# Kernel optimization log

Hardware: AMD Instinct MI355X
Metric: run time of the kernel (lower is better)

The kernel has to match this reference:

```python
import jax, jax.numpy as jnp
from jax import lax
import numpy as np

B, S, E, HID = 16, 7, 64, 64
RES = (64, 64); D = RES[0] * RES[1]
XLOW, XHIGH = -0.5, 0.5
RLOW, RHIGH = float(np.sqrt(0.01)), float(np.sqrt(0.05))
PIXEL_MULT = 1.0; N_ITER = 3; TSOFT = 1.0 / float(np.sqrt(E))

def _build_grid():
    ranges = [np.linspace(XLOW, XHIGH, r) for r in RES]
    g = np.stack(np.meshgrid(*ranges, indexing='xy'), axis=-1)
    g = g.reshape(RES[0], RES[1], -1).reshape(1, -1, 2)
    return jnp.asarray(g, dtype=jnp.float32)

ABS_GRID = _build_grid()  # [1, D, 2]

def _ln(x, g, b):
    m = jnp.mean(x, -1, keepdims=True)
    v = jnp.mean(jnp.square(x - m), -1, keepdims=True)
    return (x - m) * lax.rsqrt(v + 1e-5) * g + b

def _forward(data, slot_noise, pos_rand, conv0_w, conv0_b, conv1_w, conv1_b, conv2_w, conv2_b,
             dataN_g, dataN_b, queryN_g, queryN_b, toK_w, toK_b, toV_w, toV_b, dense_w, dense_b,
             mlp1_w, mlp1_b, mlp2_w, mlp2_b, gru_wih, gru_whh, gru_bih, gru_bhh,
             alpha1_w, alpha1_b, alpha2_w, alpha2_b, final1_w, final1_b, final2_w, final2_b,
             slots_mu, slots_logsigma):
    dn = ('NCHW', 'OIHW', 'NCHW')
    def conv(x, w, b):
        return lax.conv_general_dilated(x, w, (1, 1), 'SAME', dimension_numbers=dn) + b[None, :, None, None]
    # CNN encoder: Conv-ReLU x3, 'same' padding, k=5
    x = jax.nn.relu(conv(data, conv0_w, conv0_b))
    x = jax.nn.relu(conv(x, conv1_w, conv1_b))
    x = jax.nn.relu(conv(x, conv2_w, conv2_b))
    enc = x.transpose(0, 2, 3, 1).reshape(B, D, HID)
    enc = _ln(enc, dataN_g, dataN_b)

    queries = slots_mu + jnp.exp(slots_logsigma) * slot_noise  # [B,S,E]
    # init_slots: faithful replication (source indexes the SLOT dim, and swaps rlow/rhigh)
    pos_scale = pos_rand.at[:, :2, :].add(-0.5)
    pos_scale = pos_scale.at[:, -1, :].set((RLOW - RHIGH) * pos_rand[:, -1, :] + RHIGH)

    encK = enc @ toK_w + toK_b  # [B,D,E]
    encV = enc @ toV_w + toV_b

    def init_mlp(y):
        y = _ln(y, queryN_g, queryN_b)
        return jax.nn.relu(y @ mlp1_w + mlp1_b) @ mlp2_w + mlp2_b

    def get_kv(ps):
        # per-slot relative grid: [B,S,D,2]
        rel = (ABS_GRID[:, None] - ps[:, :, None, :2]) / ps[:, :, -1][:, :, None, None]
        eg = PIXEL_MULT * (rel @ dense_w + dense_b)  # [B,S,D,E]
        return init_mlp(encK[:, None] + eg), init_mlp(encV[:, None] + eg)

    def att_wts(q, k):
        logits = jnp.einsum('bse,bsde->bsd', q, k) * TSOFT
        att = jax.nn.softmax(logits, axis=1)  # softmax over slots
        wts = att / jnp.sum(att, -1, keepdims=True) + 1e-8
        return att, wts

    def update_frames(wts):
        new_pos = jnp.einsum('bsd,de->bse', wts, ABS_GRID[0])  # [B,S,2]
        d2 = jnp.sum(jnp.square(ABS_GRID[:, None] - new_pos[:, :, None]), -1)  # [B,S,D]
        new_scale = jnp.sqrt(jnp.einsum('bsd,bsd->bs', wts, d2))
        return jnp.concatenate([new_pos, new_scale[..., None]], -1)

    def gru(xg, h):
        gi = xg @ gru_wih.T + gru_bih
        gh = h @ gru_whh.T + gru_bhh
        ir, iz, inn = jnp.split(gi, 3, -1)
        hr, hz, hn = jnp.split(gh, 3, -1)
        r = jax.nn.sigmoid(ir + hr)
        z = jax.nn.sigmoid(iz + hz)
        n = jnp.tanh(inn + r * hn)
        return (1.0 - z) * n + z * h

    for _ in range(N_ITER):
        keys, vals = get_kv(pos_scale)
        att, wts = att_wts(_ln(queries, queryN_g, queryN_b), keys)
        pos_scale = update_frames(wts)
        upd = jnp.einsum('bsd,bsde->bse', wts, vals)
        queries = gru(upd.reshape(-1, E), queries.reshape(-1, E)).reshape(B, S, E)

    keys, _ = get_kv(pos_scale)
    att, wts = att_wts(_ln(queries, queryN_g, queryN_b), keys)
    nps = update_frames(wts)
    alpha = jax.nn.sigmoid(jax.nn.relu(queries @ alpha1_w + alpha1_b) @ alpha2_w + alpha2_b)
    slot_feat = jax.nn.relu(queries @ final1_w + final1_b) @ final2_w + final2_b + nps
    return queries, att, slot_feat, alpha

def setup_inputs() -> dict:
    ks = jax.random.split(jax.random.key(0), 20)
    f32 = jnp.float32
    def rn(i, shape, s):
        return jax.random.normal(ks[i], shape, f32) * s
    inp = dict(
        data=jax.random.normal(ks[0], (B, 1, RES[0], RES[1]), f32),
        slot_noise=jax.random.normal(ks[1], (B, S, E), f32),
        pos_rand=jax.random.uniform(ks[2], (B, S, 3), dtype=f32),
        conv0_w=rn(3, (HID, 1, 5, 5), 0.2), conv0_b=jnp.zeros(HID, f32),
        conv1_w=rn(4, (HID, HID, 5, 5), 0.025), conv1_b=jnp.zeros(HID, f32),
        conv2_w=rn(5, (HID, HID, 5, 5), 0.025), conv2_b=jnp.zeros(HID, f32),
        dataN_g=jnp.ones(HID, f32), dataN_b=jnp.zeros(HID, f32),
        queryN_g=jnp.ones(E, f32), queryN_b=jnp.zeros(E, f32),
        toK_w=rn(6, (HID, E), 0.125), toK_b=jnp.zeros(E, f32),
        toV_w=rn(7, (HID, E), 0.125), toV_b=jnp.zeros(E, f32),
        dense_w=rn(8, (2, E), 0.7), dense_b=jnp.zeros(E, f32),
        mlp1_w=rn(9, (E, E), 0.125), mlp1_b=jnp.zeros(E, f32),
        mlp2_w=rn(10, (E, E), 0.125), mlp2_b=jnp.zeros(E, f32),
        gru_wih=rn(11, (3 * E, E), 0.125), gru_whh=rn(12, (3 * E, E), 0.125),
        gru_bih=jnp.zeros(3 * E, f32), gru_bhh=jnp.zeros(3 * E, f32),
        alpha1_w=rn(13, (E, 32), 0.125), alpha1_b=jnp.zeros(32, f32),
        alpha2_w=rn(14, (32, 1), 0.18), alpha2_b=jnp.zeros(1, f32),
        final1_w=rn(15, (E, HID), 0.125), final1_b=jnp.zeros(HID, f32),
        final2_w=rn(16, (HID, 3), 0.125), final2_b=jnp.zeros(3, f32),
        slots_mu=rn(17, (1, 1, E), 1.0),
        slots_logsigma=rn(18, (1, 1, E), 0.01),
    )
    return inp

def reference(data, slot_noise, pos_rand, conv0_w, conv0_b, conv1_w, conv1_b, conv2_w, conv2_b,
              dataN_g, dataN_b, queryN_g, queryN_b, toK_w, toK_b, toV_w, toV_b, dense_w, dense_b,
              mlp1_w, mlp1_b, mlp2_w, mlp2_b, gru_wih, gru_whh, gru_bih, gru_bhh,
              alpha1_w, alpha1_b, alpha2_w, alpha2_b, final1_w, final1_b, final2_w, final2_b,
              slots_mu, slots_logsigma):
    return _forward(data, slot_noise, pos_rand, conv0_w, conv0_b, conv1_w, conv1_b, conv2_w, conv2_b,
                    dataN_g, dataN_b, queryN_g, queryN_b, toK_w, toK_b, toV_w, toV_b, dense_w, dense_b,
                    mlp1_w, mlp1_b, mlp2_w, mlp2_b, gru_wih, gru_whh, gru_bih, gru_bhh,
                    alpha1_w, alpha1_b, alpha2_w, alpha2_b, final1_w, final1_b, final2_w, final2_b,
                    slots_mu, slots_logsigma)
```

## Files before the change

kernel.cpp:

```cpp
#include <hip/hip_runtime.h>
#include <cmath>


#define RLOW_F 0.1f
#define RHIGH_F 0.22360679774997896f
#define W0CONST 1.00004096f
#define SR2 704.3386243f

typedef __attribute__((ext_vector_type(8))) __bf16 bf16x8;
typedef __attribute__((ext_vector_type(4))) float f32x4;

__device__ __forceinline__ float wsum64(float v){
  #pragma unroll
  for (int off = 32; off > 0; off >>= 1) v += __shfl_xor(v, off, 64);
  return v;
}
__device__ __forceinline__ float rdlane(float v, int l){
  return __int_as_float(__builtin_amdgcn_readlane(__float_as_int(v), l));
}
__device__ __forceinline__ unsigned short bf16bits(float v){
  __bf16 h = (__bf16)v;
  return *reinterpret_cast<unsigned short*>(&h);
}

__device__ __forceinline__ void pp_core(int row, int e, float qv,
    float px, float py, float sc,
    const float* __restrict__ qg_, const float* __restrict__ qb_,
    const float* __restrict__ dw, const float* __restrict__ db,
    const float* __restrict__ mlp2w, const float* __restrict__ mlp2b,
    float* __restrict__ absc, float* __restrict__ w2qc){
  float m = wsum64(qv) * (1.f/64.f);
  float d = qv - m;
  float var = wsum64(d*d) * (1.f/64.f);
  float qlnv = d * (1.0f/sqrtf(var + 1e-5f)) * qg_[e] + qb_[e];
  float A  = dw[e]      / sc;
  float Bv = dw[64 + e] / sc;
  absc[row*192 + e]       = A;
  absc[row*192 + 64 + e]  = Bv;
  absc[row*192 + 128 + e] = db[e] - px*A - py*Bv;
  float acc = 0.f;
  const float* wrow = mlp2w + e*64;
  for (int j = 0; j < 64; j++) acc = fmaf(wrow[j], rdlane(qlnv, j), acc);
  w2qc[row*68 + e] = acc;
  float c2 = wsum64(mlp2b[e] * qlnv);
  if (e == 0) w2qc[row*68 + 64] = c2;
}

__global__ void k_prep(const float* __restrict__ noise, const float* __restrict__ prand,
                       const float* __restrict__ mu, const float* __restrict__ logsig,
                       const float* __restrict__ qg_, const float* __restrict__ qb_,
                       const float* __restrict__ dw, const float* __restrict__ db,
                       const float* __restrict__ mlp2w, const float* __restrict__ mlp2b,
                       float* __restrict__ queries, float* __restrict__ ps,
                       float* __restrict__ absc, float* __restrict__ w2qc,
                       float* __restrict__ accF, float* __restrict__ upd){
  int row = blockIdx.x;
  int e = threadIdx.x;
  int s = row % 7;
  float qv = mu[e] + expf(logsig[e]) * noise[row*64 + e];
  queries[row*64 + e] = qv;
  upd[row*64 + e] = 0.f;
  if (e < 4) accF[row*4 + e] = 0.f;
  float pv = 0.f;
  if (e < 3){
    float pr = prand[row*3 + e];
    if (s < 2)       pv = pr - 0.5f;
    else if (s == 6) pv = (RLOW_F - RHIGH_F)*pr + RHIGH_F;
    else             pv = pr;
    ps[row*3 + e] = pv;
  }
  float px = rdlane(pv, 0), py = rdlane(pv, 1), sc = rdlane(pv, 2);
  pp_core(row, e, qv, px, py, sc, qg_, qb_, dw, db, mlp2w, mlp2b, absc, w2qc);
}

__global__ __launch_bounds__(256) void k_conv0(const float* __restrict__ in,
                        const float* __restrict__ w, const float* __restrict__ bias,
                        unsigned short* __restrict__ out){
  int bi = blockIdx.x; int b = bi >> 6; int y = bi & 63;
  int t = threadIdx.x; int lane = t & 63; int xg = t >> 6;
  __shared__ float s_in[5*68];
  __shared__ float s_w[64*25];
  __shared__ float s_out[64*65];
  for (int i = t; i < 1600; i += 256) s_w[i] = w[i];
  for (int i = t; i < 340; i += 256){
    int r = i / 68, cx = i % 68;
    int yy = y + r - 2, gx = cx - 2;
    float v = 0.f;
    if (yy >= 0 && yy < 64 && gx >= 0 && gx < 64) v = in[(b*64 + yy)*64 + gx];
    s_in[r*68 + cx] = v;
  }
  __syncthreads();
  int o = lane;
  float bvv = bias[o];
  float acc[16];
  #pragma unroll
  for (int k = 0; k < 16; k++) acc[k] = bvv;
  #pragma unroll
  for (int ky = 0; ky < 5; ky++){
    float rv[20];
    const float4* p = reinterpret_cast<const float4*>(&s_in[ky*68 + xg*16]);
    #pragma unroll
    for (int q = 0; q < 5; q++){ float4 f = p[q]; rv[q*4]=f.x; rv[q*4+1]=f.y; rv[q*4+2]=f.z; rv[q*4+3]=f.w; }
    #pragma unroll
    for (int kx = 0; kx < 5; kx++){
      float wv = s_w[o*25 + ky*5 + kx];
      #pragma unroll
      for (int k = 0; k < 16; k++) acc[k] = fmaf(rv[k+kx], wv, acc[k]);
    }
  }
  #pragma unroll
  for (int k = 0; k < 16; k++) s_out[o*65 + xg*16 + k] = fmaxf(acc[k], 0.f);
  __syncthreads();
  for (int i = t; i < 4096; i += 256){
    int px = i >> 6, ch = i & 63;
// ... 127 lines not shown
  int n = nt*16 + cr;
  out[idx] = bf16bits(w1[k*64 + n]);
}

__global__ __launch_bounds__(256) void k_projm(const float* __restrict__ enc,
                       const unsigned short* __restrict__ kpack, const float* __restrict__ bk,
                       const unsigned short* __restrict__ vpack, const float* __restrict__ bvp,
                       unsigned short* __restrict__ K, unsigned short* __restrict__ V){
  int bi = blockIdx.x; int b = bi >> 6; int tile = bi & 63;
  int t = threadIdx.x; int wv = t >> 6; int l = t & 63;
  int q = l >> 4, cr = l & 15;
  int d0 = tile*64 + wv*16;

  const bf16x8* kp = reinterpret_cast<const bf16x8*>(kpack);
  const bf16x8* vp = reinterpret_cast<const bf16x8*>(vpack);
  bf16x8 KB[8], VB[8];
  #pragma unroll
  for (int f = 0; f < 8; f++){ KB[f] = kp[f*64 + l]; VB[f] = vp[f*64 + l]; }

  const float* er = enc + (size_t)(b*4096 + d0 + cr)*64;
  bf16x8 a0, a1;
  #pragma unroll
  for (int h = 0; h < 2; h++){
    const float4* e4 = reinterpret_cast<const float4*>(er + (h ? (32 + q*8) : (q*8)));
    #pragma unroll
    for (int p = 0; p < 2; p++){
      float4 e = e4[p];
      if (h == 0){ a0[p*4+0]=(__bf16)e.x; a0[p*4+1]=(__bf16)e.y; a0[p*4+2]=(__bf16)e.z; a0[p*4+3]=(__bf16)e.w; }
      else       { a1[p*4+0]=(__bf16)e.x; a1[p*4+1]=(__bf16)e.y; a1[p*4+2]=(__bf16)e.z; a1[p*4+3]=(__bf16)e.w; }
    }
  }

  f32x4 zero = {0.f,0.f,0.f,0.f};
  f32x4 aK[4], aV[4];
  #pragma unroll
  for (int nt = 0; nt < 4; nt++){
    aK[nt] = __builtin_amdgcn_mfma_f32_16x16x32_bf16(a0, KB[nt],     zero,   0, 0, 0);
    aK[nt] = __builtin_amdgcn_mfma_f32_16x16x32_bf16(a1, KB[4 + nt], aK[nt], 0, 0, 0);
    aV[nt] = __builtin_amdgcn_mfma_f32_16x16x32_bf16(a0, VB[nt],     zero,   0, 0, 0);
    aV[nt] = __builtin_amdgcn_mfma_f32_16x16x32_bf16(a1, VB[4 + nt], aV[nt], 0, 0, 0);
  }
  #pragma unroll
  for (int nt = 0; nt < 4; nt++){
    float bkv = bk[nt*16 + cr], bvv = bvp[nt*16 + cr];
    #pragma unroll
    for (int reg = 0; reg < 4; reg++){
      size_t base = ((size_t)b*4096 + d0 + q*4 + reg)*64 + nt*16 + cr;
      K[base] = bf16bits(aK[nt][reg] + bkv);
      V[base] = bf16bits(aV[nt][reg] + bvv);
    }
  }
}

__global__ __launch_bounds__(256) void k_attnK(const unsigned short* __restrict__ encX,
     const unsigned short* __restrict__ w1pack, const float* __restrict__ mlp1b,
     const float* __restrict__ absc, const float* __restrict__ qg_,
     const float* __restrict__ qb_, const float* __restrict__ w2qc,
     float* __restrict__ att, float* __restrict__ accF){
  int bi = blockIdx.x;
  int b = bi >> 6, tile = bi & 63;
  int t = threadIdx.x; int wv = t >> 6; int l = t & 63;
  int q = l >> 4, cr = l & 15;
  int m0 = tile*64 + wv*16;
  int drow = m0 + cr;

  __shared__ float s_log[7*64];
  __shared__ float s_absc[7*192];
  __shared__ float s_wq[7*68];
  __shared__ unsigned short s_w1[4096];
  for (int i = t; i < 1344; i += 256) s_absc[i] = absc[b*7*192 + i];
  for (int i = t; i < 476;  i += 256) s_wq[i]   = w2qc[b*7*68 + i];
  {
    const uint4* g = reinterpret_cast<const uint4*>(w1pack);
    uint4* d = reinterpret_cast<uint4*>(s_w1);
    for (int i = t; i < 512; i += 256) d[i] = g[i];
  }

  const unsigned short* er = encX + (size_t)(b*4096 + drow)*64;
  float gx = -0.5f + (float)(drow & 63) * (1.f/63.f);
  float gy = -0.5f + (float)((drow >> 6) & 63) * (1.f/63.f);
  float xb[16], gq[16], bq[16];
  {
    bf16x8 ea = *reinterpret_cast<const bf16x8*>(er + q*8);
    bf16x8 eb = *reinterpret_cast<const bf16x8*>(er + 32 + q*8);
    #pragma unroll
    for (int i = 0; i < 8; i++){ xb[i] = (float)ea[i]; xb[8+i] = (float)eb[i]; }
  }
  #pragma unroll
  for (int h = 0; h < 2; h++){
    int fb = h ? (32 + q*8) : (q*8);
    const float4* g4 = reinterpret_cast<const float4*>(qg_ + fb);
    const float4* b4 = reinterpret_cast<const float4*>(qb_ + fb);
    #pragma unroll
    for (int p = 0; p < 2; p++){
      float4 gg = g4[p], bb = b4[p];
      int o = h*8 + p*4;
      gq[o+0]=gg.x; gq[o+1]=gg.y; gq[o+2]=gg.z; gq[o+3]=gg.w;
      bq[o+0]=bb.x; bq[o+1]=bb.y; bq[o+2]=bb.z; bq[o+3]=bb.w;
    }
  }
  float b1v[4];
  #pragma unroll
  for (int nt = 0; nt < 4; nt++) b1v[nt] = mlp1b[nt*16 + cr];
  __syncthreads();

  const bf16x8* wl = reinterpret_cast<const bf16x8*>(s_w1);
  f32x4 zero = {0.f, 0.f, 0.f, 0.f};

  for (int sp = 0; sp < 4; sp++){
    int s0 = sp*2;
    int np = (sp == 3) ? 1 : 2;
    int sB = (np == 2) ? s0 + 1 : s0;
    float x0[16], x1[16];
    float s1a = 0.f, s2a = 0.f, s1b = 0.f, s2b = 0.f;
    {
      const float* Ac = s_absc + s0*192;
      #pragma unroll
      for (int h = 0; h < 2; h++){
        int fb = h ? (32 + q*8) : (q*8);
        const float4* A4 = reinterpret_cast<const float4*>(Ac + fb);
        const float4* B4 = reinterpret_cast<const float4*>(Ac + 64 + fb);
        const float4* C4 = reinterpret_cast<const float4*>(Ac + 128 + fb);
        #pragma unroll
        for (int p = 0; p < 2; p++){
          float4 Av = A4[p], Bv = B4[p], Cv = C4[p];
          int o = h*8 + p*4;
          x0[o+0] = xb[o+0] + gx*Av.x + gy*Bv.x + Cv.x;
          x0[o+1] = xb[o+1] + gx*Av.y + gy*Bv.y + Cv.y;
          x0[o+2] = xb[o+2] + gx*Av.z + gy*Bv.z + Cv.z;
          x0[o+3] = xb[o+3] + gx*Av.w + gy*Bv.w + Cv.w;
        }
// ... 47 lines not shown
      bf16x8 w1f = wl[(4 + nt)*64 + l];
      acc0[nt] = __builtin_amdgcn_mfma_f32_16x16x32_bf16(a00, w0,  zero,     0, 0, 0);
      acc0[nt] = __builtin_amdgcn_mfma_f32_16x16x32_bf16(a01, w1f, acc0[nt], 0, 0, 0);
      acc1[nt] = __builtin_amdgcn_mfma_f32_16x16x32_bf16(a10, w0,  zero,     0, 0, 0);
      acc1[nt] = __builtin_amdgcn_mfma_f32_16x16x32_bf16(a11, w1f, acc1[nt], 0, 0, 0);
    }

    float p0[4] = {0.f,0.f,0.f,0.f}, p1[4] = {0.f,0.f,0.f,0.f};
    #pragma unroll
    for (int nt = 0; nt < 4; nt++){
      float wq0 = s_wq[s0*68 + nt*16 + cr];
      float wq1 = s_wq[sB*68 + nt*16 + cr];
      #pragma unroll
      for (int reg = 0; reg < 4; reg++){
        p0[reg] = fmaf(fmaxf(acc0[nt][reg] + b1v[nt], 0.f), wq0, p0[reg]);
        p1[reg] = fmaf(fmaxf(acc1[nt][reg] + b1v[nt], 0.f), wq1, p1[reg]);
      }
    }
    #pragma unroll
    for (int off = 1; off < 16; off <<= 1){
      #pragma unroll
      for (int reg = 0; reg < 4; reg++){
        p0[reg] += __shfl_xor(p0[reg], off, 64);
        p1[reg] += __shfl_xor(p1[reg], off, 64);
      }
    }
    if (cr == 0){
      float c20 = s_wq[s0*68 + 64];
      float c21 = s_wq[sB*68 + 64];
      #pragma unroll
      for (int reg = 0; reg < 4; reg++){
        s_log[s0*64 + wv*16 + q*4 + reg] = (p0[reg] + c20) * 0.125f;
        if (np == 2) s_log[sB*64 + wv*16 + q*4 + reg] = (p1[reg] + c21) * 0.125f;
      }
    }
  }
  __syncthreads();

  if (t < 64){
    float lv[7];
    #pragma unroll
    for (int s = 0; s < 7; s++) lv[s] = s_log[s*64 + t];
    float mx = lv[0];
    #pragma unroll
    for (int s = 1; s < 7; s++) mx = fmaxf(mx, lv[s]);
    float sm = 0.f;
    #pragma unroll
    for (int s = 0; s < 7; s++){ lv[s] = expf(lv[s] - mx); sm += lv[s]; }
    float inv = 1.0f / sm;
    #pragma unroll
    for (int s = 0; s < 7; s++){
      float a = lv[s] * inv;
      s_log[s*64 + t] = a;
      att[(size_t)(b*7+s)*4096 + tile*64 + t] = a;
    }
  }
  __syncthreads();

  if (t < 224){
    int s = t >> 5, r = t & 31;
    float a1 = s_log[s*64 + r];
    float a2 = s_log[s*64 + r + 32];
    float gx1 = -0.5f + (float)r * (1.f/63.f);
    float gx2 = -0.5f + (float)(r + 32) * (1.f/63.f);
    float gyc = -0.5f + (float)tile * (1.f/63.f);
    float gy2c = gyc*gyc;
    float w0 = a1 + a2;
    float w1 = a1*gx1 + a2*gx2;
    float w2 = w0*gyc;
    float w3 = a1*(gx1*gx1 + gy2c) + a2*(gx2*gx2 + gy2c);
    #pragma unroll
    for (int m = 1; m < 32; m <<= 1){
      w0 += __shfl_xor(w0, m, 64);
      w1 += __shfl_xor(w1, m, 64);
      w2 += __shfl_xor(w2, m, 64);
      w3 += __shfl_xor(w3, m, 64);
    }
    if (r == 0){
      atomicAdd(&accF[(b*7+s)*4 + 0], w0);
      atomicAdd(&accF[(b*7+s)*4 + 1], w1);
      atomicAdd(&accF[(b*7+s)*4 + 2], w2);
      atomicAdd(&accF[(b*7+s)*4 + 3], w3);
    }
  }
}

__global__ __launch_bounds__(256) void k_attnV(const unsigned short* __restrict__ encX,
     const unsigned short* __restrict__ w1pack, const float* __restrict__ mlp1b,
     const float* __restrict__ absc, const float* __restrict__ qg_,
     const float* __restrict__ qb_, const float* __restrict__ att,
     const float* __restrict__ accF, float* __restrict__ upd){
  int bi = blockIdx.x;
  int b = bi >> 6, tile = bi & 63;
  int t = threadIdx.x; int wv = t >> 6; int l = t & 63;
  int q = l >> 4, cr = l & 15;
  int m0 = tile*64 + wv*16;
  int drow = m0 + cr;

  __shared__ float s_absc[7*192];
  __shared__ float s_att[7*64];
  __shared__ float s_upd[7*64];
  __shared__ float s_inv[7];
  __shared__ unsigned short s_w1[4096];
  for (int i = t; i < 1344; i += 256) s_absc[i] = absc[b*7*192 + i];
  for (int i = t; i < 448;  i += 256){
    s_att[i] = att[(size_t)(b*7 + (i >> 6))*4096 + tile*64 + (i & 63)];
    s_upd[i] = 0.f;
  }
  if (t < 7) s_inv[t] = 1.0f / accF[(b*7 + t)*4];
  {
    const uint4* g = reinterpret_cast<const uint4*>(w1pack);
    uint4* d = reinterpret_cast<uint4*>(s_w1);
    for (int i = t; i < 512; i += 256) d[i] = g[i];
  }

  const unsigned short* er = encX + (size_t)(b*4096 + drow)*64;
  float gx = -0.5f + (float)(drow & 63) * (1.f/63.f);
  float gy = -0.5f + (float)((drow >> 6) & 63) * (1.f/63.f);
  float xb[16], gq[16], bq[16];
  {
    bf16x8 ea = *reinterpret_cast<const bf16x8*>(er + q*8);
    bf16x8 eb = *reinterpret_cast<const bf16x8*>(er + 32 + q*8);
    #pragma unroll
    for (int i = 0; i < 8; i++){ xb[i] = (float)ea[i]; xb[8+i] = (float)eb[i]; }
  }
  #pragma unroll
  for (int h = 0; h < 2; h++){
    int fb = h ? (32 + q*8) : (q*8);
    const float4* g4 = reinterpret_cast<const float4*>(qg_ + fb);
    const float4* b4 = reinterpret_cast<const float4*>(qb_ + fb);
    #pragma unroll
    for (int p = 0; p < 2; p++){
      float4 gg = g4[p], bb = b4[p];
      int o = h*8 + p*4;
      gq[o+0]=gg.x; gq[o+1]=gg.y; gq[o+2]=gg.z; gq[o+3]=gg.w;
      bq[o+0]=bb.x; bq[o+1]=bb.y; bq[o+2]=bb.z; bq[o+3]=bb.w;
    }
  }
  float b1v[4];
  #pragma unroll
  for (int nt = 0; nt < 4; nt++) b1v[nt] = mlp1b[nt*16 + cr];
  __syncthreads();

  const bf16x8* wl = reinterpret_cast<const bf16x8*>(s_w1);
  f32x4 zero = {0.f, 0.f, 0.f, 0.f};

  for (int sp = 0; sp < 4; sp++){
    int s0 = sp*2;
    int np = (sp == 3) ? 1 : 2;
    int sB = (np == 2) ? s0 + 1 : s0;
    float x0[16], x1[16];
    float s1a = 0.f, s2a = 0.f, s1b = 0.f, s2b = 0.f;
    {
      const float* Ac = s_absc + s0*192;
      #pragma unroll
      for (int h = 0; h < 2; h++){
        int fb = h ? (32 + q*8) : (q*8);
        const float4* A4 = reinterpret_cast<const float4*>(Ac + fb);
        const float4* B4 = reinterpret_cast<const float4*>(Ac + 64 + fb);
        const float4* C4 = reinterpret_cast<const float4*>(Ac + 128 + fb);
        #pragma unroll
        for (int p = 0; p < 2; p++){
          float4 Av = A4[p], Bv = B4[p], Cv = C4[p];
          int o = h*8 + p*4;
          x0[o+0] = xb[o+0] + gx*Av.x + gy*Bv.x + Cv.x;
          x0[o+1] = xb[o+1] + gx*Av.y + gy*Bv.y + Cv.y;
          x0[o+2] = xb[o+2] + gx*Av.z + gy*Bv.z + Cv.z;
          x0[o+3] = xb[o+3] + gx*Av.w + gy*Bv.w + Cv.w;
        }
      }
      #pragma unroll
      for (int k = 0; k < 16; k++){ s1a += x0[k]; s2a = fmaf(x0[k], x0[k], s2a); }
    }
    {
      const float* Ac = s_absc + sB*192;
      #pragma unroll
      for (int h = 0; h < 2; h++){
        int fb = h ? (32 + q*8) : (q*8);
        const float4* A4 = reinterpret_cast<const float4*>(Ac + fb);
        const float4* B4 = reinterpret_cast<const float4*>(Ac + 64 + fb);
        const float4* C4 = reinterpret_cast<const float4*>(Ac + 128 + fb);
        #pragma unroll
        for (int p = 0; p < 2; p++){
          float4 Av = A4[p], Bv = B4[p], Cv = C4[p];
          int o = h*8 + p*4;
          x1[o+0] = xb[o+0] + gx*Av.x + gy*Bv.x + Cv.x;
          x1[o+1] = xb[o+1] + gx*Av.y + gy*Bv.y + Cv.y;
          x1[o+2] = xb[o+2] + gx*Av.z + gy*Bv.z + Cv.z;
          x1[o+3] = xb[o+3] + gx*Av.w + gy*Bv.w + Cv.w;
        }
      }
      #pragma unroll
      for (int k = 0; k < 16; k++){ s1b += x1[k]; s2b = fmaf(x1[k], x1[k], s2b); }
    }
    s1a += __shfl_xor(s1a, 16, 64); s2a += __shfl_xor(s2a, 16, 64);
    s1b += __shfl_xor(s1b, 16, 64); s2b += __shfl_xor(s2b, 16, 64);
    s1a += __shfl_xor(s1a, 32, 64); s2a += __shfl_xor(s2a, 32, 64);
    s1b += __shfl_xor(s1b, 32, 64); s2b += __shfl_xor(s2b, 32, 64);
    float mA = s1a*(1.f/64.f);
    float rA = 1.0f/sqrtf(s2a*(1.f/64.f) - mA*mA + 1e-5f);
    float mB = s1b*(1.f/64.f);
    float rB = 1.0f/sqrtf(s2b*(1.f/64.f) - mB*mB + 1e-5f);

    bf16x8 a00, a01, a10, a11;
    #pragma unroll
    for (int k = 0; k < 8; k++){
      a00[k] = (__bf16)((x0[k]    - mA)*rA*gq[k]   + bq[k]);
      a01[k] = (__bf16)((x0[8+k]  - mA)*rA*gq[8+k] + bq[8+k]);
      a10[k] = (__bf16)((x1[k]    - mB)*rB*gq[k]   + bq[k]);
      a11[k] = (__bf16)((x1[8+k]  - mB)*rB*gq[8+k] + bq[8+k]);
    }

    f32x4 acc0[4], acc1[4];
    #pragma unroll
    for (int nt = 0; nt < 4; nt++){
      bf16x8 w0 = wl[nt*64 + l];
      bf16x8 w1f = wl[(4 + nt)*64 + l];
      acc0[nt] = __builtin_amdgcn_mfma_f32_16x16x32_bf16(a00, w0,  zero,     0, 0, 0);
      acc0[nt] = __builtin_amdgcn_mfma_f32_16x16x32_bf16(a01, w1f, acc0[nt], 0, 0, 0);
      acc1[nt] = __builtin_amdgcn_mfma_f32_16x16x32_bf16(a10, w0,  zero,     0, 0, 0);
      acc1[nt] = __builtin_amdgcn_mfma_f32_16x16x32_bf16(a11, w1f, acc1[nt], 0, 0, 0);
    }

    float rsa0 = s_inv[s0], rsa1 = s_inv[sB];
    float wr0[4], wr1[4];
    #pragma unroll
    for (int reg = 0; reg < 4; reg++){
      wr0[reg] = fmaf(s_att[s0*64 + wv*16 + q*4 + reg], rsa0, 1e-8f);
      wr1[reg] = fmaf(s_att[sB*64 + wv*16 + q*4 + reg], rsa1, 1e-8f);
    }
    float pc0[4], pc1[4];
    #pragma unroll
    for (int nt = 0; nt < 4; nt++){
      pc0[nt] = 0.f; pc1[nt] = 0.f;
      #pragma unroll
      for (int reg = 0; reg < 4; reg++){
        pc0[nt] = fmaf(wr0[reg], fmaxf(acc0[nt][reg] + b1v[nt], 0.f), pc0[nt]);
        pc1[nt] = fmaf(wr1[reg], fmaxf(acc1[nt][reg] + b1v[nt], 0.f), pc1[nt]);
      }
    }
    #pragma unroll
    for (int nt = 0; nt < 4; nt++){
      pc0[nt] += __shfl_xor(pc0[nt], 16, 64);
      pc1[nt] += __shfl_xor(pc1[nt], 16, 64);
      pc0[nt] += __shfl_xor(pc0[nt], 32, 64);
      pc1[nt] += __shfl_xor(pc1[nt], 32, 64);
    }
    if (q == 0){
      #pragma unroll
      for (int nt = 0; nt < 4; nt++){
        atomicAdd(&s_upd[s0*64 + nt*16 + cr], pc0[nt]);
        if (np == 2) atomicAdd(&s_upd[sB*64 + nt*16 + cr], pc1[nt]);
      }
    }
  }
  __syncthreads();
  for (int i = t; i < 448; i += 256)
    atomicAdd(&upd[b*448 + i], s_upd[i]);
}

__global__ void k_gru(float* __restrict__ upd, float* __restrict__ queries,
                      const float* __restrict__ wih, const float* __restrict__ whh,
                      const float* __restrict__ bih, const float* __restrict__ bhh,
                      const float* __restrict__ mlp2w, const float* __restrict__ mlp2b,
                      float* __restrict__ accF, float* __restrict__ ps,
                      const float* __restrict__ qg_, const float* __restrict__ qb_,
                      const float* __restrict__ dw, const float* __restrict__ db,
                      float* __restrict__ absc, float* __restrict__ w2qc){
  int row = blockIdx.x; int t = threadIdx.x;
  __shared__ float us[64], hs[64], xs[64], gis[192], ghs[192];
  __shared__ float s_ps3[3];
  if (t < 64){ us[t] = upd[row*64 + t]; hs[t] = queries[row*64 + t]; }
  if (t == 64){
    float sa = accF[row*4+0];
    float ax = accF[row*4+1], ay = accF[row*4+2], ar2 = accF[row*4+3];
    float isa = 1.0f/sa;
    float Wx = ax*isa, Wy = ay*isa;
    float Wg = ar2*isa + 1e-8f*SR2;
    float s2 = Wg - (Wx*Wx + Wy*Wy)*(2.f - W0CONST);
    s_ps3[0] = Wx; s_ps3[1] = Wy; s_ps3[2] = sqrtf(fmaxf(s2, 0.f));
  }
  __syncthreads();
  if (t < 64){
    float a = W0CONST * mlp2b[t];
    for (int i = 0; i < 64; i++) a = fmaf(us[i], mlp2w[i*64 + t], a);
    xs[t] = a;
  }
  __syncthreads();
  float gi = bih[t], gh = bhh[t];
  for (int e = 0; e < 64; e++){
    gi = fmaf(wih[t*64 + e], xs[e], gi);
    gh = fmaf(whh[t*64 + e], hs[e], gh);
  }
  gis[t] = gi; ghs[t] = gh;
  __syncthreads();
  if (t < 64){
    float r = 1.0f/(1.0f + expf(-(gis[t]      + ghs[t])));
    float z = 1.0f/(1.0f + expf(-(gis[64+t]   + ghs[64+t])));
    float n = tanhf(gis[128+t] + r*ghs[128+t]);
    float newq = (1.0f - z)*n + z*hs[t];
    queries[row*64 + t] = newq;
    upd[row*64 + t] = 0.f;
    if (t < 4) accF[row*4 + t] = 0.f;
    if (t < 3) ps[row*3 + t] = s_ps3[t];
    pp_core(row, t, newq, s_ps3[0], s_ps3[1], s_ps3[2],
            qg_, qb_, dw, db, mlp2w, mlp2b, absc, w2qc);
  }
}

__global__ void k_final(const float* __restrict__ queries, const float* __restrict__ accF,
                        const float* __restrict__ a1w, const float* __restrict__ a1b,
                        const float* __restrict__ a2w, const float* __restrict__ a2b,
                        const float* __restrict__ f1w, const float* __restrict__ f1b,
                        const float* __restrict__ f2w, const float* __restrict__ f2b,
                        float* __restrict__ out){
  int bs = blockIdx.x; int e = threadIdx.x;
  __shared__ float qs[64], hf[64], ha[32];
  float q = queries[bs*64 + e];
  qs[e] = q;
  out[bs*64 + e] = q;
  __syncthreads();
  float accf = f1b[e];
  for (int i = 0; i < 64; i++) accf = fmaf(qs[i], f1w[i*64 + e], accf);
  hf[e] = fmaxf(accf, 0.f);
  if (e < 32){
    float acca = a1b[e];
    for (int i = 0; i < 64; i++) acca = fmaf(qs[i], a1w[i*32 + e], acca);
    ha[e] = fmaxf(acca, 0.f);
  }
  __syncthreads();
  if (e < 3){
    float sf = f2b[e];
    for (int o = 0; o < 64; o++) sf = fmaf(hf[o], f2w[o*3 + e], sf);
    float sa = accF[bs*4+0], ax = accF[bs*4+1], ay = accF[bs*4+2], ar2 = accF[bs*4+3];
    float isa = 1.0f/sa;
    float Wx = ax*isa, Wy = ay*isa;
    float Wg = ar2*isa + 1e-8f*SR2;
    float s2 = Wg - (Wx*Wx + Wy*Wy)*(2.f - W0CONST);
    float nv = (e == 0) ? Wx : ((e == 1) ? Wy : sqrtf(fmaxf(s2, 0.f)));
    out[465920 + bs*3 + e] = sf + nv;
  }
  if (e == 32){
    float al = a2b[0];
    for (int o = 0; o < 32; o++) al = fmaf(ha[o], a2w[o], al);
    out[466256 + bs] = 1.0f/(1.0f + expf(-al));
  }
}

extern "C" void kernel_launch(void* const* d_in, const int* in_sizes, int n_in,
                              void* d_out, int out_size, void* d_ws, size_t ws_size,
                              hipStream_t stream){
  const float* data        = (const float*)d_in[0];
  const float* slot_noise  = (const float*)d_in[1];
  const float* pos_rand    = (const float*)d_in[2];
  const float* conv0_w     = (const float*)d_in[3];
  const float* conv0_b     = (const float*)d_in[4];
  const float* conv1_w     = (const float*)d_in[5];
  const float* conv1_b     = (const float*)d_in[6];
  const float* conv2_w     = (const float*)d_in[7];
  const float* conv2_b     = (const float*)d_in[8];
  const float* dataN_g     = (const float*)d_in[9];
  const float* dataN_b     = (const float*)d_in[10];
  const float* queryN_g    = (const float*)d_in[11];
  const float* queryN_b    = (const float*)d_in[12];
  const float* toK_w       = (const float*)d_in[13];
  const float* toK_b       = (const float*)d_in[14];
  const float* toV_w       = (const float*)d_in[15];
  const float* toV_b       = (const float*)d_in[16];
  const float* dense_w     = (const float*)d_in[17];
  const float* dense_b     = (const float*)d_in[18];
  const float* mlp1_w      = (const float*)d_in[19];
  const float* mlp1_b      = (const float*)d_in[20];
  const float* mlp2_w      = (const float*)d_in[21];
  const float* mlp2_b      = (const float*)d_in[22];
  const float* gru_wih     = (const float*)d_in[23];
  const float* gru_whh     = (const float*)d_in[24];
  const float* gru_bih     = (const float*)d_in[25];
  const float* gru_bhh     = (const float*)d_in[26];
  const float* alpha1_w    = (const float*)d_in[27];
  const float* alpha1_b    = (const float*)d_in[28];
  const float* alpha2_w    = (const float*)d_in[29];
  const float* alpha2_b    = (const float*)d_in[30];
  const float* final1_w    = (const float*)d_in[31];
  const float* final1_b    = (const float*)d_in[32];
  const float* final2_w    = (const float*)d_in[33];
  const float* final2_b    = (const float*)d_in[34];
  const float* slots_mu    = (const float*)d_in[35];
  const float* slots_lsig  = (const float*)d_in[36];

  float* ws   = (float*)d_ws;
  float* bufA = ws;
  float* bufB = bufA + 4194304;
  float* bufC = bufB + 4194304;
  float* attw = bufC + 4194304;
  float* queries = attw + 458752;
  float* ps   = queries + 7168;
  float* absc = ps + 512;
  float* accF = absc + 21504;
  float* upd  = accF + 512;
  float* w2qc = upd + 7168;
  unsigned short* w1pack = (unsigned short*)(w2qc + 7616);
  unsigned short* kpack  = w1pack + 4096;
  unsigned short* vpack  = kpack + 4096;
  unsigned short* wp1    = vpack + 4096;
  unsigned short* wp2    = wp1 + 102400;

  unsigned short* c0_bf = (unsigned short*)bufA;
  unsigned short* c1_bf = (unsigned short*)bufC;
  float* enc = bufB;
  unsigned short* encK = (unsigned short*)bufA;
  unsigned short* encV = (unsigned short*)bufC;

  float* outq   = (float*)d_out;
  float* outatt = outq + 7168;

  k_prep<<<112, 64, 0, stream>>>(slot_noise, pos_rand, slots_mu, slots_lsig,
                                 queryN_g, queryN_b, dense_w, dense_b, mlp2_w, mlp2_b,
                                 queries, ps, absc, w2qc, accF, upd);
  k_packw1<<<16, 256, 0, stream>>>(mlp1_w, w1pack);
  k_packw1<<<16, 256, 0, stream>>>(toK_w, kpack);
  k_packw1<<<16, 256, 0, stream>>>(toV_w, vpack);
  k_packconv<<<400, 256, 0, stream>>>(conv1_w, wp1);
  k_packconv<<<400, 256, 0, stream>>>(conv2_w, wp2);
  k_conv0<<<1024, 256, 0, stream>>>(data, conv0_w, conv0_b, c0_bf);
  k_convm<<<256, 256, 0, stream>>>(c0_bf, wp1, conv1_b, nullptr, nullptr, c1_bf, nullptr, 0);
  k_convm<<<256, 256, 0, stream>>>(c1_bf, wp2, conv2_b, dataN_g, dataN_b, nullptr, enc, 1);
  k_projm<<<1024, 256, 0, stream>>>(enc, kpack, toK_b, vpack, toV_b, encK, encV);

  for (int p = 0; p < 4; p++){
    float* attp = (p == 3) ? outatt : attw;
    k_attnK<<<1024, 256, 0, stream>>>(encK, w1pack, mlp1_b, absc, queryN_g, queryN_b,
                                      w2qc, attp, accF);
    if (p < 3){
      k_attnV<<<1024, 256, 0, stream>>>(encV, w1pack, mlp1_b, absc, queryN_g, queryN_b,
                                        attp, accF, upd);
      k_gru<<<112, 192, 0, stream>>>(upd, queries, gru_wih, gru_whh, gru_bih, gru_bhh,
                                     mlp2_w, mlp2_b, accF, ps, queryN_g, queryN_b,
                                     dense_w, dense_b, absc, w2qc);
    }
  }
  k_final<<<112, 64, 0, stream>>>(queries, accF,
                                  alpha1_w, alpha1_b, alpha2_w, alpha2_b,
                                  final1_w, final1_b, final2_w, final2_b, outq);
}
```

Measured before the change: 526.2 us.

## Fuse attention-logit and value-aggregation kernels using deferred normalization

Merges the key-side softmax kernel and the value-aggregation kernel into a single kernel per iteration. The per-slot normalisation by the attention sum is deferred: the kernel accumulates sum(a*y) and sum(y) separately, and the GRU kernel later combines them as gp1/sum + 1e-8*gp2. This removes one launch per iteration, the global attention write and re-read, and the second staging of weights and absc. In exchange each fused block carries more registers and shared memory, and it does two global atomic reductions instead of one.

Measured after the change: 539.8 us. 2.6% more time.

```diff
diff --git a/kernel.cpp b/kernel.cpp
--- a/kernel.cpp
+++ b/kernel.cpp
@@ -53,13 +53,15 @@
                        const float* __restrict__ mlp2w, const float* __restrict__ mlp2b,
                        float* __restrict__ queries, float* __restrict__ ps,
                        float* __restrict__ absc, float* __restrict__ w2qc,
-                       float* __restrict__ accF, float* __restrict__ upd){
+                       float* __restrict__ accF,
+                       float* __restrict__ gp1, float* __restrict__ gp2){
   int row = blockIdx.x;
   int e = threadIdx.x;
   int s = row % 7;
   float qv = mu[e] + expf(logsig[e]) * noise[row*64 + e];
   queries[row*64 + e] = qv;
-  upd[row*64 + e] = 0.f;
+  gp1[row*64 + e] = 0.f;
+  gp2[row*64 + e] = 0.f;
   if (e < 4) accF[row*4 + e] = 0.f;
   float pv = 0.f;
   if (e < 3){
@@ -293,11 +295,13 @@
   }
 }
 
-__global__ __launch_bounds__(256) void k_attnK(const unsigned short* __restrict__ encX,
+__global__ __launch_bounds__(256) void k_attn(const unsigned short* __restrict__ encK,
+     const unsigned short* __restrict__ encV,
      const unsigned short* __restrict__ w1pack, const float* __restrict__ mlp1b,
      const float* __restrict__ absc, const float* __restrict__ qg_,
      const float* __restrict__ qb_, const float* __restrict__ w2qc,
-     float* __restrict__ att, float* __restrict__ accF){
+     float* __restrict__ att, float* __restrict__ accF,
+     float* __restrict__ gp1, float* __restrict__ gp2, int mode){
   int bi = blockIdx.x;
   int b = bi >> 6, tile = bi & 63;
   int t = threadIdx.x; int wv = t >> 6; int l = t & 63;
@@ -308,16 +312,21 @@
   __shared__ float s_log[7*64];
   __shared__ float s_absc[7*192];
   __shared__ float s_wq[7*68];
+  __shared__ float s_up1[7*64];
+  __shared__ float s_up2[7*64];
   __shared__ unsigned short s_w1[4096];
   for (int i = t; i < 1344; i += 256) s_absc[i] = absc[b*7*192 + i];
   for (int i = t; i < 476;  i += 256) s_wq[i]   = w2qc[b*7*68 + i];
+  if (mode == 0){
+    for (int i = t; i < 448; i += 256){ s_up1[i] = 0.f; s_up2[i] = 0.f; }
+  }
   {
     const uint4* g = reinterpret_cast<const uint4*>(w1pack);
     uint4* d = reinterpret_cast<uint4*>(s_w1);
     for (int i = t; i < 512; i += 256) d[i] = g[i];
   }
 
-  const unsigned short* er = encX + (size_t)(b*4096 + drow)*64;
+  const unsigned short* er = encK + (size_t)(b*4096 + drow)*64;
   float gx = -0.5f + (float)(drow & 63) * (1.f/63.f);
   float gy = -0.5f + (float)((drow >> 6) & 63) * (1.f/63.f);
   float xb[16], gq[16], bq[16];
@@ -471,7 +480,7 @@
     for (int s = 0; s < 7; s++){
       float a = lv[s] * inv;
       s_log[s*64 + t] = a;
-      att[(size_t)(b*7+s)*4096 + tile*64 + t] = a;
+      if (mode == 1) att[(size_t)(b*7+s)*4096 + tile*64 + t] = a;
     }
   }
   __syncthreads();
@@ -502,183 +511,146 @@
       atomicAdd(&accF[(b*7+s)*4 + 3], w3);
     }
   }
-}
-
-__global__ __launch_bounds__(256) void k_attnV(const unsigned short* __restrict__ encX,
-     const unsigned short* __restrict__ w1pack, const float* __restrict__ mlp1b,
-     const float* __restrict__ absc, const float* __restrict__ qg_,
-     const float* __restrict__ qb_, const float* __restrict__ att,
-     const float* __restrict__ accF, float* __restrict__ upd){
-  int bi = blockIdx.x;
-  int b = bi >> 6, tile = bi & 63;
-  int t = threadIdx.x; int wv = t >> 6; int l = t & 63;
-  int q = l >> 4, cr = l & 15;
-  int m0 = tile*64 + wv*16;
-  int drow = m0 + cr;
-
-  __shared__ float s_absc[7*192];
-  __shared__ float s_att[7*64];
-  __shared__ float s_upd[7*64];
-  __shared__ float s_inv[7];
-  __shared__ unsigned short s_w1[4096];
-  for (int i = t; i < 1344; i += 256) s_absc[i] = absc[b*7*192 + i];
-  for (int i = t; i < 448;  i += 256){
-    s_att[i] = att[(size_t)(b*7 + (i >> 6))*4096 + tile*64 + (i & 63)];
-    s_upd[i] = 0.f;
-  }
-  if (t < 7) s_inv[t] = 1.0f / accF[(b*7 + t)*4];
-  {
-    const uint4* g = reinterpret_cast<const uint4*>(w1pack);
-    uint4* d = reinterpret_cast<uint4*>(s_w1);
-    for (int i = t; i < 512; i += 256) d[i] = g[i];
-  }
-
-  const unsigned short* er = encX + (size_t)(b*4096 + drow)*64;
-  float gx = -0.5f + (float)(drow & 63) * (1.f/63.f);
-  float gy = -0.5f + (float)((drow >> 6) & 63) * (1.f/63.f);
-  float xb[16], gq[16], bq[16];
-  {
-    bf16x8 ea = *reinterpret_cast<const bf16x8*>(er + q*8);
-    bf16x8 eb = *reinterpret_cast<const bf16x8*>(er + 32 + q*8);
-    #pragma unroll
-    for (int i = 0; i < 8; i++){ xb[i] = (float)ea[i]; xb[8+i] = (float)eb[i]; }
-  }
-  #pragma unroll
-  for (int h = 0; h < 2; h++){
-    int fb = h ? (32 + q*8) : (q*8);
-    const float4* g4 = reinterpret_cast<const float4*>(qg_ + fb);
-    const float4* b4 = reinterpret_cast<const float4*>(qb_ + fb);
-    #pragma unroll
-    for (int p = 0; p < 2; p++){
-      float4 gg = g4[p], bb = b4[p];
-      int o = h*8 + p*4;
-      gq[o+0]=gg.x; gq[o+1]=gg.y; gq[o+2]=gg.z; gq[o+3]=gg.w;
-      bq[o+0]=bb.x; bq[o+1]=bb.y; bq[o+2]=bb.z; bq[o+3]=bb.w;
-    }
-  }
-  float b1v[4];
-  #pragma unroll
-  for (int nt = 0; nt < 4; nt++) b1v[nt] = mlp1b[nt*16 + cr];
-  __syncthreads();
-
-  const bf16x8* wl = reinterpret_cast<const bf16x8*>(s_w1);
-  f32x4 zero = {0.f, 0.f, 0.f, 0.f};
-
-  for (int sp = 0; sp < 4; sp++){
-    int s0 = sp*2;
-    int np = (sp == 3) ? 1 : 2;
-    int sB = (np == 2) ? s0 + 1 : s0;
-    float x0[16], x1[16];
-    float s1a = 0.f, s2a = 0.f, s1b = 0.f, s2b = 0.f;
+
+  if (mode == 0){
+    float vb[16];
     {
-      const float* Ac = s_absc + s0*192;
-      #pragma unroll
-      for (int h = 0; h < 2; h++){
-        int fb = h ? (32 + q*8) : (q*8);
-        const float4* A4 = reinterpret_cast<const float4*>(Ac + fb);
-        const float4* B4 = reinterpret_cast<const float4*>(Ac + 64 + fb);
-        const float4* C4 = reinterpret_cast<const float4*>(Ac + 128 + fb);
-        #pragma unroll
-        for (int p = 0; p < 2; p++){
-          float4 Av = A4[p], Bv = B4[p], Cv = C4[p];
-          int o = h*8 + p*4;
-          x0[o+0] = xb[o+0] + gx*Av.x + gy*Bv.x + Cv.x;
-          x0[o+1] = xb[o+1] + gx*Av.y + gy*Bv.y + Cv.y;
-          x0[o+2] = xb[o+2] + gx*Av.z + gy*Bv.z + Cv.z;
-          x0[o+3] = xb[o+3] + gx*Av.w + gy*Bv.w + Cv.w;
+      const unsigned short* ev = encV + (size_t)(b*4096 + drow)*64;
+      bf16x8 ea = *reinterpret_cast<const bf16x8*>(ev + q*8);
+      bf16x8 eb = *reinterpret_cast<const bf16x8*>(ev + 32 + q*8);
+      #pragma unroll
+      for (int i = 0; i < 8; i++){ vb[i] = (float)ea[i]; vb[8+i] = (float)eb[i]; }
+    }
+    for (int sp = 0; sp < 4; sp++){
+      int s0 = sp*2;
+      int np = (sp == 3) ? 1 : 2;
+      int sB = (np == 2) ? s0 + 1 : s0;
+      float x0[16], x1[16];
+      float s1a = 0.f, s2a = 0.f, s1b = 0.f, s2b = 0.f;
+      {
+        const float* Ac = s_absc + s0*192;
+        #pragma unroll
+        for (int h = 0; h < 2; h++){
+          int fb = h ? (32 + q*8) : (q*8);
+          const float4* A4 = reinterpret_cast<const float4*>(Ac + fb);
+          const float4* B4 = reinterpret_cast<const float4*>(Ac + 64 + fb);
+          const float4* C4 = reinterpret_cast<const float4*>(Ac + 128 + fb);
+          #pragma unroll
+          for (int p = 0; p < 2; p++){
+            float4 Av = A4[p], Bv = B4[p], Cv = C4[p];
+            int o = h*8 + p*4;
+            x0[o+0] = vb[o+0] + gx*Av.x + gy*Bv.x + Cv.x;
+            x0[o+1] = vb[o+1] + gx*Av.y + gy*Bv.y + Cv.y;
+            x0[o+2] = vb[o+2] + gx*Av.z + gy*Bv.z + Cv.z;
+            x0[o+3] = vb[o+3] + gx*Av.w + gy*Bv.w + Cv.w;
+          }
         }
-      }
-      #pragma unroll
-      for (int k = 0; k < 16; k++){ s1a += x0[k]; s2a = fmaf(x0[k], x0[k], s2a); }
-    }
-    {
-      const float* Ac = s_absc + sB*192;
-      #pragma unroll
-      for (int h = 0; h < 2; h++){
-        int fb = h ? (32 + q*8) : (q*8);
-        const float4* A4 = reinterpret_cast<const float4*>(Ac + fb);
-        const float4* B4 = reinterpret_cast<const float4*>(Ac + 64 + fb);
-        const float4* C4 = reinterpret_cast<const float4*>(Ac + 128 + fb);
-        #pragma unroll
-        for (int p = 0; p < 2; p++){
-          float4 Av = A4[p], Bv = B4[p], Cv = C4[p];
-          int o = h*8 + p*4;
-          x1[o+0] = xb[o+0] + gx*Av.x + gy*Bv.x + Cv.x;
-          x1[o+1] = xb[o+1] + gx*Av.y + gy*Bv.y + Cv.y;
-          x1[o+2] = xb[o+2] + gx*Av.z + gy*Bv.z + Cv.z;
-          x1[o+3] = xb[o+3] + gx*Av.w + gy*Bv.w + Cv.w;
+        #pragma unroll
+        for (int k = 0; k < 16; k++){ s1a += x0[k]; s2a = fmaf(x0[k], x0[k], s2a); }
+      }
+      {
+        const float* Ac = s_absc + sB*192;
+        #pragma unroll
+        for (int h = 0; h < 2; h++){
+          int fb = h ? (32 + q*8) : (q*8);
+          const float4* A4 = reinterpret_cast<const float4*>(Ac + fb);
+          const float4* B4 = reinterpret_cast<const float4*>(Ac + 64 + fb);
+          const float4* C4 = reinterpret_cast<const float4*>(Ac + 128 + fb);
+          #pragma unroll
+          for (int p = 0; p < 2; p++){
+            float4 Av = A4[p], Bv = B4[p], Cv = C4[p];
+            int o = h*8 + p*4;
+            x1[o+0] = vb[o+0] + gx*Av.x + gy*Bv.x + Cv.x;
+            x1[o+1] = vb[o+1] + gx*Av.y + gy*Bv.y + Cv.y;
+            x1[o+2] = vb[o+2] + gx*Av.z + gy*Bv.z + Cv.z;
+            x1[o+3] = vb[o+3] + gx*Av.w + gy*Bv.w + Cv.w;
+          }
         }
-      }
-      #pragma unroll
-      for (int k = 0; k < 16; k++){ s1b += x1[k]; s2b = fmaf(x1[k], x1[k], s2b); }
-    }
-    s1a += __shfl_xor(s1a, 16, 64); s2a += __shfl_xor(s2a, 16, 64);
-    s1b += __shfl_xor(s1b, 16, 64); s2b += __shfl_xor(s2b, 16, 64);
-    s1a += __shfl_xor(s1a, 32, 64); s2a += __shfl_xor(s2a, 32, 64);
-    s1b += __shfl_xor(s1b, 32, 64); s2b += __shfl_xor(s2b, 32, 64);
-    float mA = s1a*(1.f/64.f);
-    float rA = 1.0f/sqrtf(s2a*(1.f/64.f) - mA*mA + 1e-5f);
-    float mB = s1b*(1.f/64.f);
-    float rB = 1.0f/sqrtf(s2b*(1.f/64.f) - mB*mB + 1e-5f);
-
-    bf16x8 a00, a01, a10, a11;
-    #pragma unroll
-    for (int k = 0; k < 8; k++){
-      a00[k] = (__bf16)((x0[k]    - mA)*rA*gq[k]   + bq[k]);
-      a01[k] = (__bf16)((x0[8+k]  - mA)*rA*gq[8+k] + bq[8+k]);
-      a10[k] = (__bf16)((x1[k]    - mB)*rB*gq[k]   + bq[k]);
-      a11[k] = (__bf16)((x1[8+k]  - mB)*rB*gq[8+k] + bq[8+k]);
-    }
-
-    f32x4 acc0[4], acc1[4];
-    #pragma unroll
-    for (int nt = 0; nt < 4; nt++){
-      bf16x8 w0 = wl[nt*64 + l];
-      bf16x8 w1f = wl[(4 + nt)*64 + l];
-      acc0[nt] = __builtin_amdgcn_mfma_f32_16x16x32_bf16(a00, w0,  zero,     0, 0, 0);
-      acc0[nt] = __builtin_amdgcn_mfma_f32_16x16x32_bf16(a01, w1f, acc0[nt], 0, 0, 0);
-      acc1[nt] = __builtin_amdgcn_mfma_f32_16x16x32_bf16(a10, w0,  zero,     0, 0, 0);
-      acc1[nt] = __builtin_amdgcn_mfma_f32_16x16x32_bf16(a11, w1f, acc1[nt], 0, 0, 0);
-    }
-
-    float rsa0 = s_inv[s0], rsa1 = s_inv[sB];
-    float wr0[4], wr1[4];
-    #pragma unroll
-    for (int reg = 0; reg < 4; reg++){
-      wr0[reg] = fmaf(s_att[s0*64 + wv*16 + q*4 + reg], rsa0, 1e-8f);
-      wr1[reg] = fmaf(s_att[sB*64 + wv*16 + q*4 + reg], rsa1, 1e-8f);
-    }
-    float pc0[4], pc1[4];
-    #pragma unroll
-    for (int nt = 0; nt < 4; nt++){
-      pc0[nt] = 0.f; pc1[nt] = 0.f;
+        #pragma unroll
+        for (int k = 0; k < 16; k++){ s1b += x1[k]; s2b = fmaf(x1[k], x1[k], s2b); }
+      }
+      s1a += __shfl_xor(s1a, 16, 64); s2a += __shfl_xor(s2a, 16, 64);
+      s1b += __shfl_xor(s1b, 16, 64); s2b += __shfl_xor(s2b, 16, 64);
+      s1a += __shfl_xor(s1a, 32, 64); s2a += __shfl_xor(s2a, 32, 64);
+      s1b += __shfl_xor(s1b, 32, 64); s2b += __shfl_xor(s2b, 32, 64);
+      float mA = s1a*(1.f/64.f);
+      float rA = 1.0f/sqrtf(s2a*(1.f/64.f) - mA*mA + 1e-5f);
+      float mB = s1b*(1.f/64.f);
+      float rB = 1.0f/sqrtf(s2b*(1.f/64.f) - mB*mB + 1e-5f);
+
+      bf16x8 a00, a01, a10, a11;
+      #pragma unroll
+      for (int k = 0; k < 8; k++){
+        a00[k] = (__bf16)((x0[k]    - mA)*rA*gq[k]   + bq[k]);
+        a01[k] = (__bf16)((x0[8+k]  - mA)*rA*gq[8+k] + bq[8+k]);
+        a10[k] = (__bf16)((x1[k]    - mB)*rB*gq[k]   + bq[k]);
+        a11[k] = (__bf16)((x1[8+k]  - mB)*rB*gq[8+k] + bq[8+k]);
+      }
+
+      f32x4 acc0[4], acc1[4];
+      #pragma unroll
+      for (int nt = 0; nt < 4; nt++){
+        bf16x8 w0 = wl[nt*64 + l];
+        bf16x8 w1f = wl[(4 + nt)*64 + l];
+        acc0[nt] = __builtin_amdgcn_mfma_f32_16x16x32_bf16(a00, w0,  zero,     0, 0, 0);
+        acc0[nt] = __builtin_amdgcn_mfma_f32_16x16x32_bf16(a01, w1f, acc0[nt], 0, 0, 0);
+        acc1[nt] = __builtin_amdgcn_mfma_f32_16x16x32_bf16(a10, w0,  zero,     0, 0, 0);
+        acc1[nt] = __builtin_amdgcn_mfma_f32_16x16x32_bf16(a11, w1f, acc1[nt], 0, 0, 0);
+      }
+
+      float wr0[4], wr1[4];
       #pragma unroll
       for (int reg = 0; reg < 4; reg++){
-        pc0[nt] = fmaf(wr0[reg], fmaxf(acc0[nt][reg] + b1v[nt], 0.f), pc0[nt]);
-        pc1[nt] = fmaf(wr1[reg], fmaxf(acc1[nt][reg] + b1v[nt], 0.f), pc1[nt]);
-      }
-    }
-    #pragma unroll
-    for (int nt = 0; nt < 4; nt++){
-      pc0[nt] += __shfl_xor(pc0[nt], 16, 64);
-      pc1[nt] += __shfl_xor(pc1[nt], 16, 64);
-      pc0[nt] += __shfl_xor(pc0[nt], 32, 64);
-      pc1[nt] += __shfl_xor(pc1[nt], 32, 64);
-    }
-    if (q == 0){
+        wr0[reg] = s_log[s0*64 + wv*16 + q*4 + reg];
+        wr1[reg] = s_log[sB*64 + wv*16 + q*4 + reg];
+      }
+      float pa0[4], pb0[4], pa1[4], pb1[4];
       #pragma unroll
       for (int nt = 0; nt < 4; nt++){
-        atomicAdd(&s_upd[s0*64 + nt*16 + cr], pc0[nt]);
-        if (np == 2) atomicAdd(&s_upd[sB*64 + nt*16 + cr], pc1[nt]);
-      }
-    }
-  }
-  __syncthreads();
-  for (int i = t; i < 448; i += 256)
-    atomicAdd(&upd[b*448 + i], s_upd[i]);
-}
-
-__global__ void k_gru(float* __restrict__ upd, float* __restrict__ queries,
+        pa0[nt] = 0.f; pb0[nt] = 0.f; pa1[nt] = 0.f; pb1[nt] = 0.f;
+        #pragma unroll
+        for (int reg = 0; reg < 4; reg++){
+          float y0 = fmaxf(acc0[nt][reg] + b1v[nt], 0.f);
+          float y1 = fmaxf(acc1[nt][reg] + b1v[nt], 0.f);
+          pa0[nt] = fmaf(wr0[reg], y0, pa0[nt]);
+          pb0[nt] += y0;
+          pa1[nt] = fmaf(wr1[reg], y1, pa1[nt]);
+          pb1[nt] += y1;
+        }
+      }
+      #pragma unroll
+      for (int nt = 0; nt < 4; nt++){
+        pa0[nt] += __shfl_xor(pa0[nt], 16, 64);
+        pb0[nt] += __shfl_xor(pb0[nt], 16, 64);
+        pa1[nt] += __shfl_xor(pa1[nt], 16, 64);
+        pb1[nt] += __shfl_xor(pb1[nt], 16, 64);
+        pa0[nt] += __shfl_xor(pa0[nt], 32, 64);
+        pb0[nt] += __shfl_xor(pb0[nt], 32, 64);
+        pa1[nt] += __shfl_xor(pa1[nt], 32, 64);
+        pb1[nt] += __shfl_xor(pb1[nt], 32, 64);
+      }
+      if (q == 0){
+        #pragma unroll
+        for (int nt = 0; nt < 4; nt++){
+          atomicAdd(&s_up1[s0*64 + nt*16 + cr], pa0[nt]);
+          atomicAdd(&s_up2[s0*64 + nt*16 + cr], pb0[nt]);
+          if (np == 2){
+            atomicAdd(&s_up1[sB*64 + nt*16 + cr], pa1[nt]);
+            atomicAdd(&s_up2[sB*64 + nt*16 + cr], pb1[nt]);
+          }
+        }
+      }
+    }
+    __syncthreads();
+    for (int i = t; i < 448; i += 256){
+      atomicAdd(&gp1[b*448 + i], s_up1[i]);
+      atomicAdd(&gp2[b*448 + i], s_up2[i]);
+    }
+  }
+}
+
+__global__ void k_gru(float* __restrict__ gp1, float* __restrict__ gp2,
+                      float* __restrict__ queries,
                       const float* __restrict__ wih, const float* __restrict__ whh,
                       const float* __restrict__ bih, const float* __restrict__ bhh,
                       const float* __restrict__ mlp2w, const float* __restrict__ mlp2b,
@@ -689,7 +661,14 @@
   int row = blockIdx.x; int t = threadIdx.x;
   __shared__ float us[64], hs[64], xs[64], gis[192], ghs[192];
   __shared__ float s_ps3[3];
-  if (t < 64){ us[t] = upd[row*64 + t]; hs[t] = queries[row*64 + t]; }
+  if (t < 64){
+    float sa = accF[row*4 + 0];
+    float isa = 1.0f/sa;
+    us[t] = gp1[row*64 + t]*isa + 1e-8f*gp2[row*64 + t];
+    gp1[row*64 + t] = 0.f;
+    gp2[row*64 + t] = 0.f;
+    hs[t] = queries[row*64 + t];
+  }
   if (t == 64){
     float sa = accF[row*4+0];
     float ax = accF[row*4+1], ay = accF[row*4+2], ar2 = accF[row*4+3];
@@ -719,7 +698,6 @@
     float n = tanhf(gis[128+t] + r*ghs[128+t]);
     float newq = (1.0f - z)*n + z*hs[t];
     queries[row*64 + t] = newq;
-    upd[row*64 + t] = 0.f;
     if (t < 4) accF[row*4 + t] = 0.f;
     if (t < 3) ps[row*3 + t] = s_ps3[t];
     pp_core(row, t, newq, s_ps3[0], s_ps3[1], s_ps3[2],
@@ -811,13 +789,13 @@
   float* bufA = ws;
   float* bufB = bufA + 4194304;
   float* bufC = bufB + 4194304;
-  float* attw = bufC + 4194304;
-  float* queries = attw + 458752;
+  float* queries = bufC + 4194304;
   float* ps   = queries + 7168;
   float* absc = ps + 512;
   float* accF = absc + 21504;
-  float* upd  = accF + 512;
-  float* w2qc = upd + 7168;
+  float* gp1  = accF + 512;
+  float* gp2  = gp1 + 7168;
+  float* w2qc = gp2 + 7168;
   unsigned short* w1pack = (unsigned short*)(w2qc + 7616);
   unsigned short* kpack  = w1pack + 4096;
   unsigned short* vpack  = kpack + 4096;
@@ -835,7 +813,7 @@
 
   k_prep<<<112, 64, 0, stream>>>(slot_noise, pos_rand, slots_mu, slots_lsig,
                                  queryN_g, queryN_b, dense_w, dense_b, mlp2_w, mlp2_b,
-                                 queries, ps, absc, w2qc, accF, upd);
+                                 queries, ps, absc, w2qc, accF, gp1, gp2);
   k_packw1<<<16, 256, 0, stream>>>(mlp1_w, w1pack);
   k_packw1<<<16, 256, 0, stream>>>(toK_w, kpack);
   k_packw1<<<16, 256, 0, stream>>>(toV_w, vpack);
@@ -846,18 +824,18 @@
   k_convm<<<256, 256, 0, stream>>>(c1_bf, wp2, conv2_b, dataN_g, dataN_b, nullptr, enc, 1);
   k_projm<<<1024, 256, 0, stream>>>(enc, kpack, toK_b, vpack, toV_b, encK, encV);
 
-  for (int p = 0; p < 4; p++){
-    float* attp = (p == 3) ? outatt : attw;
-    k_attnK<<<1024, 256, 0, stream>>>(encK, w1pack, mlp1_b, absc, queryN_g, queryN_b,
-                                      w2qc, attp, accF);
-    if (p < 3){
-      k_attnV<<<1024, 256, 0, stream>>>(encV, w1pack, mlp1_b, absc, queryN_g, queryN_b,
-                                        attp, accF, upd);
-      k_gru<<<112, 192, 0, stream>>>(upd, queries, gru_wih, gru_whh, gru_bih, gru_bhh,
-                                     mlp2_w, mlp2_b, accF, ps, queryN_g, queryN_b,
-                                     dense_w, dense_b, absc, w2qc);
-    }
-  }
+  for (int p = 0; p < 3; p++){
+    k_attn<<<1024, 256, 0, stream>>>(encK, encV, w1pack, mlp1_b, absc,
+                                     queryN_g, queryN_b, w2qc,
+                                     outatt, accF, gp1, gp2, 0);
+    k_gru<<<112, 192, 0, stream>>>(gp1, gp2, queries,
+                                   gru_wih, gru_whh, gru_bih, gru_bhh,
+                                   mlp2_w, mlp2_b, accF, ps, queryN_g, queryN_b,
+                                   dense_w, dense_b, absc, w2qc);
+  }
+  k_attn<<<1024, 256, 0, stream>>>(encK, encV, w1pack, mlp1_b, absc,
+                                   queryN_g, queryN_b, w2qc,
+                                   outatt, accF, gp1, gp2, 1);
   k_final<<<112, 64, 0, stream>>>(queries, accF,
                                   alpha1_w, alpha1_b, alpha2_w, alpha2_b,
                                   final1_w, final1_b, final2_w, final2_b, outq);
```
